# Optimization experiments

Measured on AMD Instinct MI355X. Metric: run time of the kernel, lower is better.

The kernel has to match this reference:

```python
import math
import jax, jax.numpy as jnp
import numpy as np

OLEN = 512
RATIO = 0.5
DROP_P = 0.2


def _gat(x, src, dst, W, a_s, a_d, b):
    """PyG GATConv (heads=1, concat=True, add_self_loops=True, neg_slope=0.2)."""
    n = x.shape[0]
    loops = jnp.arange(n, dtype=src.dtype)
    s = jnp.concatenate([src, loops])  # [E+N] source nodes
    d = jnp.concatenate([dst, loops])  # [E+N] destination nodes
    h = x @ W                           # [N, H]
    alpha_s = h @ a_s                   # [N]
    alpha_d = h @ a_d                   # [N]
    e = jax.nn.leaky_relu(alpha_s[s] + alpha_d[d], 0.2)  # [E+N]
    # segment softmax over destination neighborhoods
    m = jax.ops.segment_max(e, d, num_segments=n)
    ee = jnp.exp(e - m[d])
    denom = jax.ops.segment_sum(ee, d, num_segments=n)
    alpha = ee / denom[d]
    out = jax.ops.segment_sum(alpha[:, None] * h[s], d, num_segments=n)
    return out + b


def _forward(x, src, dst, W1, a_src1, a_dst1, b1, W2, a_src2, a_dst2, b2,
             W3, a_src3, a_dst3, b3, W_rel, W_root, b_pool):
    N, E = x.shape[0], src.shape[0]
    key = jax.random.key(42)
    h = x
    for i, (W, a_s, a_d, b) in enumerate([(W1, a_src1, a_dst1, b1),
                                          (W2, a_src2, a_dst2, b2),
                                          (W3, a_src3, a_dst3, b3)]):
        h = jax.nn.relu(_gat(h, src, dst, W, a_s, a_d, b))
        keep = jax.random.bernoulli(jax.random.fold_in(key, i), 1.0 - DROP_P, h.shape)
        h = jnp.where(keep, h / (1.0 - DROP_P), 0.0)  # F.dropout(training=True)

    # SAGPooling(GraphConv score, ratio=0.5, tanh) repeated until n <= 512.
    # Node counts are static per iteration (k = ceil(0.5*n)); edge arrays keep
    # fixed size E with a validity mask (edges dropped when an endpoint is pooled away).
    cur_src, cur_dst = src, dst
    emask = jnp.ones((E,), dtype=h.dtype)
    n = N
    while True:
        agg = jax.ops.segment_sum(h[cur_src] * emask[:, None], cur_dst, num_segments=n)
        score = (agg @ W_rel + h @ W_root + b_pool)[:, 0]  # GraphConv(d->1), aggr='add'
        score = jnp.tanh(score)
        k = math.ceil(RATIO * n)
        top_vals, perm = jax.lax.top_k(score, k)
        h = h[perm] * top_vals[:, None]
        inv = jnp.full((n,), -1, dtype=cur_src.dtype).at[perm].set(
            jnp.arange(k, dtype=cur_src.dtype))
        ns, nd = inv[cur_src], inv[cur_dst]
        valid = (ns >= 0) & (nd >= 0)
        emask = emask * valid.astype(emask.dtype)
        cur_src = jnp.where(valid, ns, 0)
        cur_dst = jnp.where(valid, nd, 0)
        n = k
        if n <= OLEN:
            break

    out = jnp.zeros((OLEN, h.shape[1]), h.dtype).at[:n].set(h)
    return out


def setup_inputs() -> dict:
    key = jax.random.key(0)
    ks = jax.random.split(key, 20)
    N, E, IDIM, HDIM = 50000, 800000, 128, 200
    inp = {
        "x": jax.random.normal(ks[0], (N, IDIM), jnp.float32),
        "src": jax.random.randint(ks[1], (E,), 0, N, jnp.int32),
        "dst": jax.random.randint(ks[2], (E,), 0, N, jnp.int32),
    }
    def w(k, shape, fan_in):
        return jax.random.normal(k, shape, jnp.float32) / np.sqrt(fan_in).astype(np.float32)
    inp["W1"] = w(ks[3], (IDIM, HDIM), IDIM)
    inp["a_src1"] = w(ks[4], (HDIM,), HDIM)
    inp["a_dst1"] = w(ks[5], (HDIM,), HDIM)
    inp["b1"] = jnp.zeros((HDIM,), jnp.float32)
    inp["W2"] = w(ks[6], (HDIM, HDIM), HDIM)
    inp["a_src2"] = w(ks[7], (HDIM,), HDIM)
    inp["a_dst2"] = w(ks[8], (HDIM,), HDIM)
    inp["b2"] = jnp.zeros((HDIM,), jnp.float32)
    inp["W3"] = w(ks[9], (HDIM, HDIM), HDIM)
    inp["a_src3"] = w(ks[10], (HDIM,), HDIM)
    inp["a_dst3"] = w(ks[11], (HDIM,), HDIM)
    inp["b3"] = jnp.zeros((HDIM,), jnp.float32)
    inp["W_rel"] = w(ks[12], (HDIM, 1), HDIM)
    inp["W_root"] = w(ks[13], (HDIM, 1), HDIM)
    inp["b_pool"] = jnp.zeros((1,), jnp.float32)
    return inp


def reference(x, src, dst, W1, a_src1, a_dst1, b1, W2, a_src2, a_dst2, b2,
              W3, a_src3, a_dst3, b3, W_rel, W_root, b_pool):
    return _forward(x, src, dst, W1, a_src1, a_dst1, b1, W2, a_src2, a_dst2, b2,
                    W3, a_src3, a_dst3, b3, W_rel, W_root, b_pool)
```

## Files before the change

### kernel.cpp

```cpp
#include <hip/hip_runtime.h>
#include <cstdint>
#include <cstddef>


__host__ __device__ inline void tf_round(uint32_t &x0, uint32_t &x1, int r) {
  x0 += x1;
  x1 = (x1 << r) | (x1 >> (32 - r));
  x1 ^= x0;
}

__host__ __device__ inline void threefry2x32(uint32_t k0, uint32_t k1,
                                             uint32_t &x0, uint32_t &x1) {
  uint32_t ks2 = k0 ^ k1 ^ 0x1BD11BDAu;
  x0 += k0; x1 += k1;
  tf_round(x0, x1, 13); tf_round(x0, x1, 15); tf_round(x0, x1, 26); tf_round(x0, x1, 6);
  x0 += k1; x1 += ks2 + 1u;
  tf_round(x0, x1, 17); tf_round(x0, x1, 29); tf_round(x0, x1, 16); tf_round(x0, x1, 24);
  x0 += ks2; x1 += k0 + 2u;
  tf_round(x0, x1, 13); tf_round(x0, x1, 15); tf_round(x0, x1, 26); tf_round(x0, x1, 6);
  x0 += k0; x1 += k1 + 3u;
  tf_round(x0, x1, 17); tf_round(x0, x1, 29); tf_round(x0, x1, 16); tf_round(x0, x1, 24);
  x0 += k1; x1 += ks2 + 4u;
  tf_round(x0, x1, 13); tf_round(x0, x1, 15); tf_round(x0, x1, 26); tf_round(x0, x1, 6);
  x0 += ks2; x1 += k0 + 5u;
}

__global__ __launch_bounds__(256) void gemm200_k(
    const float* __restrict__ A, const float* __restrict__ B,
    float* __restrict__ C, int M, int K) {
  __shared__ __align__(16) float As[128 * 8];
  __shared__ __align__(16) float Bs[8][208];
  int tid = threadIdx.x;
  int m0 = blockIdx.x * 128;
  int r = tid >> 2;
  int colBase = (tid & 3) * 52;
  float acc0[52], acc1[52];
#pragma unroll
  for (int q = 0; q < 52; q++) { acc0[q] = 0.f; acc1[q] = 0.f; }

  for (int k0 = 0; k0 < K; k0 += 8) {
    {
      int row = tid >> 1;
      int c = (tid & 1) * 4;
      int gm = m0 + row;
      float4 v = make_float4(0.f, 0.f, 0.f, 0.f);
      if (gm < M) v = *(const float4*)(A + (size_t)gm * K + (k0 + c));
      *(float4*)(&As[row * 8 + c]) = v;
    }
    for (int t = tid; t < 400; t += 256) {
      int kk = t / 50;
      int c = (t - kk * 50) * 4;
      *(float4*)(&Bs[kk][c]) = *(const float4*)(B + (size_t)(k0 + kk) * 200 + c);
    }
    __syncthreads();
#pragma unroll
    for (int kk = 0; kk < 8; kk++) {
      float a0 = As[r * 8 + kk];
      float a1 = As[(r + 64) * 8 + kk];
#pragma unroll
      for (int q = 0; q < 13; q++) {
        float4 b = *(const float4*)(&Bs[kk][colBase + 4 * q]);
        acc0[4 * q + 0] += a0 * b.x; acc0[4 * q + 1] += a0 * b.y;
        acc0[4 * q + 2] += a0 * b.z; acc0[4 * q + 3] += a0 * b.w;
        acc1[4 * q + 0] += a1 * b.x; acc1[4 * q + 1] += a1 * b.y;
        acc1[4 * q + 2] += a1 * b.z; acc1[4 * q + 3] += a1 * b.w;
      }
    }
    __syncthreads();
  }
  int gm0 = m0 + r, gm1 = m0 + r + 64;
#pragma unroll
  for (int q = 0; q < 52; q++) {
    int col = colBase + q;
    if (col < 200) {
      if (gm0 < M) C[(size_t)gm0 * 200 + col] = acc0[q];
      if (gm1 < M) C[(size_t)gm1 * 200 + col] = acc1[q];
    }
  }
}

__global__ __launch_bounds__(256) void dual_dot_k(
    const float* __restrict__ H, const float* __restrict__ v1,
    const float* __restrict__ v2, float* __restrict__ o1,
    float* __restrict__ o2, int n) {
  int wave = blockIdx.x * 4 + (threadIdx.x >> 6);
  int lane = threadIdx.x & 63;
  if (wave >= n) return;
  const float* row = H + (size_t)wave * 200;
  float s1 = 0.f, s2 = 0.f;
  for (int d = lane; d < 200; d += 64) {
    float h = row[d];
    s1 += h * v1[d];
    s2 += h * v2[d];
  }
  for (int off = 32; off; off >>= 1) {
    s1 += __shfl_down(s1, off);
    s2 += __shfl_down(s2, off);
  }
  if (lane == 0) { o1[wave] = s1; o2[wave] = s2; }
}

__global__ __launch_bounds__(256) void indeg_k(const int* __restrict__ dst,
                                               int* __restrict__ cnt, int E) {
  int e = blockIdx.x * 256 + threadIdx.x;
  if (e < E) atomicAdd(&cnt[dst[e]], 1);
}

__global__ __launch_bounds__(256) void scan_k(const int* __restrict__ cnt,
                                              int* __restrict__ rowptr, int N) {
  __shared__ int psum[256];
  int t = threadIdx.x;
  int CH = (N + 255) / 256;
  int beg = t * CH, end = min(beg + CH, N);
  if (beg > N) { beg = N; }
  int s = 0;
  for (int i = beg; i < end; i++) s += cnt[i];
  psum[t] = s;
  __syncthreads();
  if (t == 0) {
    int run = 0;
    for (int i = 0; i < 256; i++) { int v = psum[i]; psum[i] = run; run += v; }
  }
  __syncthreads();
  int run = psum[t];
  for (int i = beg; i < end; i++) { rowptr[i] = run; run += cnt[i]; }
  if (end == N && beg <= N) rowptr[N] = run;
}

__global__ __launch_bounds__(256) void cpyint_k(const int* __restrict__ a,
                                                int* __restrict__ b, int n) {
  int i = blockIdx.x * 256 + threadIdx.x;
  if (i < n) b[i] = a[i];
}

__global__ __launch_bounds__(256) void place_k(const int* __restrict__ dst,
                                               int* __restrict__ curs,
                                               int* __restrict__ csr, int E) {
  int e = blockIdx.x * 256 + threadIdx.x;
  if (e >= E) return;
  int pos = atomicAdd(&curs[dst[e]], 1);
  csr[pos] = e;
}

__global__ __launch_bounds__(256) void sortrow_k(const int* __restrict__ rowptr,
                                                 int* __restrict__ csr, int N) {
  int d = blockIdx.x * 256 + threadIdx.x;
  if (d >= N) return;
  int b = rowptr[d], e2 = rowptr[d + 1];
  for (int i = b + 1; i < e2; i++) {
    int v = csr[i];
    int j = i - 1;
    while (j >= b && csr[j] > v) { csr[j + 1] = csr[j]; j--; }
    csr[j + 1] = v;
  }
}

__device__ inline float dec_ord(unsigned enc) {
  unsigned b = (enc & 0x80000000u) ? (enc ^ 0x80000000u) : ~enc;
  return __uint_as_float(b);
}

__global__ __launch_bounds__(256) void edge_max_k(
    const int* __restrict__ src, const int* __restrict__ dst,
    const float* __restrict__ as_, const float* __restrict__ ad_,
    unsigned* __restrict__ menc, int E, int N) {
  int j = blockIdx.x * 256 + threadIdx.x;
  if (j >= E + N) return;
  int s, d;
  if (j < E) { s = src[j]; d = dst[j]; } else { s = j - E; d = s; }
  float v = as_[s] + ad_[d];
  float ev = (v >= 0.f) ? v : 0.2f * v;
  unsigned b = __float_as_uint(ev);
  unsigned enc = (b & 0x80000000u) ? ~b : (b | 0x80000000u);
  atomicMax(&menc[d], enc);
}

__global__ __launch_bounds__(256) void ee_k(
    const int* __restrict__ src, const int* __restrict__ dst,
    const float* __restrict__ as_, const float* __restrict__ ad_,
    const unsigned* __restrict__ menc, float* __restrict__ ee, int E, int N) {
  int j = blockIdx.x * 256 + threadIdx.x;
  if (j >= E + N) return;
  int s, d;
  if (j < E) { s = src[j]; d = dst[j]; } else { s = j - E; d = s; }
  float v = as_[s] + ad_[d];
  float ev = (v >= 0.f) ? v : 0.2f * v;
  ee[j] = expf(ev - dec_ord(menc[d]));
}

__global__ __launch_bounds__(256) void den_k(const int* __restrict__ rowptr,
                                             const int* __restrict__ csr,
                                             const float* __restrict__ ee,
                                             float* __restrict__ den, int E, int N) {
  int d = blockIdx.x * 256 + threadIdx.x;
  if (d >= N) return;
  float s = 0.f;
  int b = rowptr[d], e2 = rowptr[d + 1];
  for (int i = b; i < e2; i++) s = __fadd_rn(s, ee[csr[i]]);
  s = __fadd_rn(s, ee[E + d]);
  den[d] = s;
}

__global__ __launch_bounds__(256) void alpha_k(const int* __restrict__ dst,
                                               const float* __restrict__ den,
                                               float* __restrict__ ee, int E, int N) {
  int j = blockIdx.x * 256 + threadIdx.x;
  if (j >= E + N) return;
  int d = (j < E) ? dst[j] : (j - E);
  ee[j] = ee[j] / den[d];
}

__global__ __launch_bounds__(256) void gat_out_k(
    const int* __restrict__ rowptr, const int* __restrict__ csr,
    const int* __restrict__ src, const float* __restrict__ alpha,
    const float* __restrict__ HW, float* __restrict__ OUT, int E, int N) {
  int node = blockIdx.x * 4 + (threadIdx.x >> 6);
  int lane = threadIdx.x & 63;
  if (node >= N || lane >= 50) return;
  float4 acc = make_float4(0.f, 0.f, 0.f, 0.f);
  int b = rowptr[node], e2 = rowptr[node + 1];
  for (int i = b; i < e2; i++) {
    int e = csr[i];
    int s = src[e];
    float w = alpha[e];
    float4 hv = *(const float4*)(HW + (size_t)s * 200 + 4 * lane);
    acc.x = __fadd_rn(acc.x, __fmul_rn(w, hv.x));
    acc.y = __fadd_rn(acc.y, __fmul_rn(w, hv.y));
    acc.z = __fadd_rn(acc.z, __fmul_rn(w, hv.z));
    acc.w = __fadd_rn(acc.w, __fmul_rn(w, hv.w));
  }
  {
    float w = alpha[E + node];
    float4 hv = *(const float4*)(HW + (size_t)node * 200 + 4 * lane);
    acc.x = __fadd_rn(acc.x, __fmul_rn(w, hv.x));
    acc.y = __fadd_rn(acc.y, __fmul_rn(w, hv.y));
    acc.z = __fadd_rn(acc.z, __fmul_rn(w, hv.z));
    acc.w = __fadd_rn(acc.w, __fmul_rn(w, hv.w));
  }
  *(float4*)(OUT + (size_t)node * 200 + 4 * lane) = acc;
}

__global__ __launch_bounds__(256) void epi_k(float* __restrict__ H,
                                             const float* __restrict__ bias,
                                             uint32_t k0, uint32_t k1, int total) {
  int t = blockIdx.x * 256 + threadIdx.x;
  if (t >= total) return;
  uint32_t x0 = 0u, x1 = (uint32_t)t;
  threefry2x32(k0, k1, x0, x1);
  uint32_t bits = x0 ^ x1;
  float u = __uint_as_float((bits >> 9) | 0x3f800000u) - 1.0f;
  int col = t % 200;
  float v = H[t] + bias[col];
  v = fmaxf(v, 0.f);
  H[t] = (u < 0.8f) ? (v / 0.8f) : 0.f;
}

__global__ __launch_bounds__(256) void einit_k(
    const int* __restrict__ src, const int* __restrict__ dst,
    int* __restrict__ cs, int* __restrict__ cd, int* __restrict__ orig,
    int E, int N) {
  int e = blockIdx.x * 256 + threadIdx.x;
  if (e < E) { cs[e] = src[e]; cd[e] = dst[e]; }
  if (e < N) orig[e] = e;
}

__global__ __launch_bounds__(256) void pool_agg_k(
    const int* __restrict__ rowptr, const int* __restrict__ csr,
    const int* __restrict__ csrc, const int* __restrict__ orig,
    const float* __restrict__ H, float* __restrict__ AGG, int n) {
  int node = blockIdx.x * 4 + (threadIdx.x >> 6);
  int lane = threadIdx.x & 63;
  if (node >= n || lane >= 50) return;
  int o = orig[node];
  float4 acc = make_float4(0.f, 0.f, 0.f, 0.f);
  int b = rowptr[o], e2 = rowptr[o + 1];
  for (int i = b; i < e2; i++) {
    int e = csr[i];
    int s = csrc[e];
    if (s < 0) continue;
    float4 hv = *(const float4*)(H + (size_t)s * 200 + 4 * lane);
    acc.x = __fadd_rn(acc.x, hv.x);
    acc.y = __fadd_rn(acc.y, hv.y);
    acc.z = __fadd_rn(acc.z, hv.z);
    acc.w = __fadd_rn(acc.w, hv.w);
  }
  *(float4*)(AGG + (size_t)node * 200 + 4 * lane) = acc;
}

__global__ __launch_bounds__(256) void score2_k(
    const float* __restrict__ AGG, const float* __restrict__ H,
    const float* __restrict__ wrel, const float* __restrict__ wroot,
    const float* __restrict__ bp, float* __restrict__ score, int n) {
  int node = blockIdx.x * 4 + (threadIdx.x >> 6);
  int lane = threadIdx.x & 63;
  if (node >= n) return;
  const float* arow = AGG + (size_t)node * 200;
  const float* hrow = H + (size_t)node * 200;
  float s1 = 0.f, s2 = 0.f;
  for (int d = lane; d < 200; d += 64) {
    s1 += arow[d] * wrel[d];
    s2 += hrow[d] * wroot[d];
  }
  for (int off = 32; off; off >>= 1) {
    s1 += __shfl_down(s1, off);
    s2 += __shfl_down(s2, off);
  }
  if (lane == 0) score[node] = tanhf((s1 + s2) + bp[0]);
}

__global__ __launch_bounds__(256) void rank_k(const float* __restrict__ score,
                                              int* __restrict__ rank, int n) {
  __shared__ float sc[256];
  int i = blockIdx.x * 256 + threadIdx.x;
  int nseg = gridDim.y, seg = blockIdx.y;
  int jbeg = (int)(((long long)n * seg) / nseg);
  int jend = (int)(((long long)n * (seg + 1)) / nseg);
  float si = (i < n) ? score[i] : 0.f;
  int cnt = 0;
  for (int base = jbeg; base < jend; base += 256) {
    int j = base + threadIdx.x;
    sc[threadIdx.x] = (j < jend) ? score[j] : 0.f;
    __syncthreads();
    int lim = min(256, jend - base);
#pragma unroll 8
    for (int t = 0; t < lim; t++) {
      float sj = sc[t];
      cnt += ((sj > si) || (sj == si && (base + t) < i)) ? 1 : 0;
    }
    __syncthreads();
  }
  if (i < n) atomicAdd(&rank[i], cnt);
}

__global__ __launch_bounds__(256) void perm_inv_k(const int* __restrict__ rank,
                                                  int* __restrict__ perm,
                                                  int* __restrict__ inv,
                                                  int n, int k) {
  int i = blockIdx.x * 256 + threadIdx.x;
  if (i >= n) return;
  int r = rank[i];
  if (r < k) { perm[r] = i; inv[i] = r; }
  else inv[i] = -1;
}

__global__ __launch_bounds__(256) void orig_update_k(const int* __restrict__ perm,
                                                     const int* __restrict__ oin,
                                                     int* __restrict__ oout, int k) {
  int r = blockIdx.x * 256 + threadIdx.x;
  if (r < k) oout[r] = oin[perm[r]];
}

__global__ __launch_bounds__(256) void gather_k(
    const float* __restrict__ H, const int* __restrict__ perm,
    const float* __restrict__ score, float* __restrict__ Ho, int k) {
  int r = blockIdx.x;
  int d = threadIdx.x;
  int p = perm[r];
  float s = score[p];
  if (d < 200) Ho[(size_t)r * 200 + d] = __fmul_rn(H[(size_t)p * 200 + d], s);
}

__global__ __launch_bounds__(256) void remap_k(int* __restrict__ cs,
                                               int* __restrict__ cd,
                                               const int* __restrict__ inv, int E) {
  int e = blockIdx.x * 256 + threadIdx.x;
  if (e >= E) return;
  int a = cs[e];
  if (a < 0) return;
  int na = inv[a], nb = inv[cd[e]];
  bool valid = (na >= 0) && (nb >= 0);
  cs[e] = valid ? na : -1;
  cd[e] = valid ? nb : -1;
}

__global__ __launch_bounds__(256) void out_copy_k(const float* __restrict__ h,
                                                  float* __restrict__ out, int cnt) {
  int t = blockIdx.x * 256 + threadIdx.x;
  if (t < cnt) out[t] = h[t];
}

extern "C" void kernel_launch(void* const* d_in, const int* in_sizes, int n_in,
                              void* d_out, int out_size, void* d_ws, size_t ws_size,
                              hipStream_t stream) {
  const int ID = 128, HD = 200;
  const int N = in_sizes[0] / ID;
  const int E = in_sizes[1];
  const int ET = E + N;
  const int total = N * HD;

  const float* x = (const float*)d_in[0];
  const int* src = (const int*)d_in[1];
  const int* dst = (const int*)d_in[2];
  const float* W[3]   = {(const float*)d_in[3], (const float*)d_in[7], (const float*)d_in[11]};
  const float* asv[3] = {(const float*)d_in[4], (const float*)d_in[8], (const float*)d_in[12]};
  const float* adv[3] = {(const float*)d_in[5], (const float*)d_in[9], (const float*)d_in[13]};
  const float* bv[3]  = {(const float*)d_in[6], (const float*)d_in[10], (const float*)d_in[14]};
  const float* Wrel  = (const float*)d_in[15];
  const float* Wroot = (const float*)d_in[16];
  const float* bpool = (const float*)d_in[17];

  char* ws = (char*)d_ws;
  float*    bufA  = (float*)(ws + 0);
  float*    bufB  = (float*)(ws + 40000000);
  float*    as_   = (float*)(ws + 80000000);
  float*    ad_   = (float*)(ws + 80200000);
  float*    ee_   = (float*)(ws + 80400000);
  unsigned* menc  = (unsigned*)(ws + 83800000);
  float*    den   = (float*)(ws + 84000000);
  float*    score = (float*)(ws + 84200000);
  int*      rank_ = (int*)(ws + 84400000);
  int*      perm_ = (int*)(ws + 84600000);
  int*      inv_  = (int*)(ws + 84800000);
  int*      origA = (int*)(ws + 85000000);
  int*      origB = (int*)(ws + 85200000);
  int*      rowptr= (int*)(ws + 85400000);
  int*      curs  = (int*)(ws + 85650000);
  int*      csr   = (int*)(ws + 85850000);
  int*      csrc  = (int*)(ws + 89050000);
  int*      cdst  = (int*)(ws + 92250000);

  uint32_t fk0[3], fk1[3];
  for (int i = 0; i < 3; i++) {
    uint32_t a = 0u, b = (uint32_t)i;
    threefry2x32(0u, 42u, a, b);
    fk0[i] = a; fk1[i] = b;
  }

  const int B256 = 256;
  hipMemsetAsync(rank_, 0, (size_t)N * 4, stream);
  indeg_k<<<(E + 255) / 256, B256, 0, stream>>>(dst, rank_, E);
  scan_k<<<1, B256, 0, stream>>>(rank_, rowptr, N);
  cpyint_k<<<(N + 255) / 256, B256, 0, stream>>>(rowptr, curs, N);
  place_k<<<(E + 255) / 256, B256, 0, stream>>>(dst, curs, csr, E);
  sortrow_k<<<(N + 255) / 256, B256, 0, stream>>>(rowptr, csr, N);

  for (int i = 0; i < 3; i++) {
    const float* in = (i == 0) ? x : bufB;
    int K = (i == 0) ? ID : HD;
    gemm200_k<<<(N + 127) / 128, B256, 0, stream>>>(in, W[i], bufA, N, K);
    dual_dot_k<<<(N + 3) / 4, B256, 0, stream>>>(bufA, asv[i], adv[i], as_, ad_, N);
    hipMemsetAsync(menc, 0, (size_t)N * 4, stream);
    edge_max_k<<<(ET + 255) / 256, B256, 0, stream>>>(src, dst, as_, ad_, menc, E, N);
    ee_k<<<(ET + 255) / 256, B256, 0, stream>>>(src, dst, as_, ad_, menc, ee_, E, N);
    den_k<<<(N + 255) / 256, B256, 0, stream>>>(rowptr, csr, ee_, den, E, N);
    alpha_k<<<(ET + 255) / 256, B256, 0, stream>>>(dst, den, ee_, E, N);
    gat_out_k<<<(N + 3) / 4, B256, 0, stream>>>(rowptr, csr, src, ee_, bufA, bufB, E, N);
    epi_k<<<(total + 255) / 256, B256, 0, stream>>>(bufB, bv[i], fk0[i], fk1[i], total);
  }

  einit_k<<<(E + 255) / 256, B256, 0, stream>>>(src, dst, csrc, cdst, origA, E, N);
  float* hcur = bufB;
  float* hnext = bufA;
  int* ocur = origA;
  int* onext = origB;
  int n = N;
  while (true) {
    int k = (n + 1) / 2;
    pool_agg_k<<<(n + 3) / 4, B256, 0, stream>>>(rowptr, csr, csrc, ocur, hcur, hnext, n);
    score2_k<<<(n + 3) / 4, B256, 0, stream>>>(hnext, hcur, Wrel, Wroot, bpool, score, n);
    hipMemsetAsync(rank_, 0, (size_t)n * 4, stream);
    {
      dim3 grid((n + 255) / 256, 8);
      rank_k<<<grid, B256, 0, stream>>>(score, rank_, n);
    }
    perm_inv_k<<<(n + 255) / 256, B256, 0, stream>>>(rank_, perm_, inv_, n, k);
    orig_update_k<<<(k + 255) / 256, B256, 0, stream>>>(perm_, ocur, onext, k);
    gather_k<<<k, B256, 0, stream>>>(hcur, perm_, score, hnext, k);
    remap_k<<<(E + 255) / 256, B256, 0, stream>>>(csrc, cdst, inv_, E);
    { float* t = hcur; hcur = hnext; hnext = t; }
    { int* t = ocur; ocur = onext; onext = t; }
    n = k;
    if (n <= 512) break;
  }

  hipMemsetAsync(d_out, 0, (size_t)out_size * 4, stream);
  out_copy_k<<<(n * HD + 255) / 256, B256, 0, stream>>>(hcur, (float*)d_out, n * HD);
}
```

Before: 2.830 ms.

## Replace quadratic pairwise rank with 16-bit radix bucketing for top-k

The O(n^2) all-pairs comparison used to rank pooling scores is replaced by a bucket scheme. Each score becomes an order-preserving descending key, is histogrammed on its top 16 bits, the histogram is prefix-scanned, nodes are scattered into buckets, and each node's rank is computed by comparing only within its own bucket. Ties are broken by node index, as before. This removes the quadratic work but adds four small launches, a single-block scan, and atomics, and within-bucket cost can degrade if many tanh scores share the same high bits.

```diff
diff --git a/kernel.cpp b/kernel.cpp
--- a/kernel.cpp
+++ b/kernel.cpp
@@ -308,28 +308,74 @@
   if (lane == 0) score[node] = tanhf((s1 + s2) + bp[0]);
 }
 
-__global__ __launch_bounds__(256) void rank_k(const float* __restrict__ score,
-                                              int* __restrict__ rank, int n) {
-  __shared__ float sc[256];
+__device__ inline unsigned desc_key(float f) {
+  if (f == 0.0f) f = 0.0f;
+  unsigned u = __float_as_uint(f);
+  unsigned e = (u & 0x80000000u) ? ~u : (u | 0x80000000u);
+  return ~e;
+}
+
+__global__ __launch_bounds__(256) void binc_k(const float* __restrict__ score,
+                                              unsigned* __restrict__ dkey,
+                                              int* __restrict__ hist, int n) {
   int i = blockIdx.x * 256 + threadIdx.x;
-  int nseg = gridDim.y, seg = blockIdx.y;
-  int jbeg = (int)(((long long)n * seg) / nseg);
-  int jend = (int)(((long long)n * (seg + 1)) / nseg);
-  float si = (i < n) ? score[i] : 0.f;
-  int cnt = 0;
-  for (int base = jbeg; base < jend; base += 256) {
-    int j = base + threadIdx.x;
-    sc[threadIdx.x] = (j < jend) ? score[j] : 0.f;
-    __syncthreads();
-    int lim = min(256, jend - base);
-#pragma unroll 8
-    for (int t = 0; t < lim; t++) {
-      float sj = sc[t];
-      cnt += ((sj > si) || (sj == si && (base + t) < i)) ? 1 : 0;
-    }
-    __syncthreads();
-  }
-  if (i < n) atomicAdd(&rank[i], cnt);
+  if (i >= n) return;
+  unsigned d = desc_key(score[i]);
+  dkey[i] = d;
+  atomicAdd(&hist[d >> 16], 1);
+}
+
+__global__ __launch_bounds__(256) void scanh_k(const int* __restrict__ hist,
+                                               int* __restrict__ binstart,
+                                               int* __restrict__ cursor) {
+  __shared__ int psum[256];
+  int t = threadIdx.x;
+  int base = t * 256;
+  int s = 0;
+  for (int i = 0; i < 256; i++) s += hist[base + i];
+  psum[t] = s;
+  __syncthreads();
+  if (t == 0) {
+    int run = 0;
+    for (int i = 0; i < 256; i++) { int v = psum[i]; psum[i] = run; run += v; }
+  }
+  __syncthreads();
+  int run = psum[t];
+  for (int i = 0; i < 256; i++) {
+    binstart[base + i] = run;
+    cursor[base + i] = run;
+    run += hist[base + i];
+  }
+}
+
+__global__ __launch_bounds__(256) void bplace_k(const unsigned* __restrict__ dkey,
+                                                int* __restrict__ cursor,
+                                                int* __restrict__ bucket, int n) {
+  int i = blockIdx.x * 256 + threadIdx.x;
+  if (i >= n) return;
+  int pos = atomicAdd(&cursor[dkey[i] >> 16], 1);
+  bucket[pos] = i;
+}
+
+__global__ __launch_bounds__(256) void brank_k(const unsigned* __restrict__ dkey,
+                                               const int* __restrict__ binstart,
+                                               const int* __restrict__ hist,
+                                               const int* __restrict__ bucket,
+                                               int* __restrict__ rank, int n) {
+  int i = blockIdx.x * 256 + threadIdx.x;
+  if (i >= n) return;
+  unsigned d = dkey[i];
+  int b = d >> 16;
+  int lo = binstart[b];
+  int hi = lo + hist[b];
+  unsigned long long my = ((unsigned long long)d << 20) | (unsigned)i;
+  int cnt = lo;
+  for (int m = lo; m < hi; m++) {
+    int j = bucket[m];
+    unsigned long long K = ((unsigned long long)dkey[j] << 20) | (unsigned)j;
+    cnt += (K < my) ? 1 : 0;
+  }
+  rank[i] = cnt;
 }
 
 __global__ __launch_bounds__(256) void perm_inv_k(const int* __restrict__ rank,
@@ -419,6 +465,12 @@
   int*      csrc  = (int*)(ws + 89050000);
   int*      cdst  = (int*)(ws + 92250000);
 
+  int*      hist     = (int*)ee_;
+  int*      binstart = (int*)ee_ + 65536;
+  int*      cursor   = (int*)ee_ + 131072;
+  int*      bucket   = (int*)menc;
+  unsigned* dkey     = (unsigned*)den;
+
   uint32_t fk0[3], fk1[3];
   for (int i = 0; i < 3; i++) {
     uint32_t a = 0u, b = (uint32_t)i;
@@ -458,11 +510,11 @@
     int k = (n + 1) / 2;
     pool_agg_k<<<(n + 3) / 4, B256, 0, stream>>>(rowptr, csr, csrc, ocur, hcur, hnext, n);
     score2_k<<<(n + 3) / 4, B256, 0, stream>>>(hnext, hcur, Wrel, Wroot, bpool, score, n);
-    hipMemsetAsync(rank_, 0, (size_t)n * 4, stream);
-    {
-      dim3 grid((n + 255) / 256, 8);
-      rank_k<<<grid, B256, 0, stream>>>(score, rank_, n);
-    }
+    hipMemsetAsync(hist, 0, 65536 * 4, stream);
+    binc_k<<<(n + 255) / 256, B256, 0, stream>>>(score, dkey, hist, n);
+    scanh_k<<<1, B256, 0, stream>>>(hist, binstart, cursor);
+    bplace_k<<<(n + 255) / 256, B256, 0, stream>>>(dkey, cursor, bucket, n);
+    brank_k<<<(n + 255) / 256, B256, 0, stream>>>(dkey, binstart, hist, bucket, rank_, n);
     perm_inv_k<<<(n + 255) / 256, B256, 0, stream>>>(rank_, perm_, inv_, n, k);
     orig_update_k<<<(k + 255) / 256, B256, 0, stream>>>(perm_, ocur, onext, k);
     gather_k<<<k, B256, 0, stream>>>(hcur, perm_, score, hnext, k);
```

Result: slower. 6.285 ms (+122.1%).
